# Kernel optimization log

Measured on AMD Instinct MI355X. Metric: run time of the kernel, lower is better.

Reference implementation:

```python
import jax, jax.numpy as jnp
import numpy as np

B, S, E = 4, 1024, 1280
H = 16
D = E // H  # 80


def rotate_half(x):
    x1, x2 = jnp.split(x, 2, axis=-1)
    return jnp.concatenate([-x2, x1], axis=-1)


def setup_inputs() -> dict:
    key = jax.random.key(0)
    ks = jax.random.split(key, 12)
    sc = 0.02
    x = jax.random.normal(ks[0], (B, S, E), dtype=jnp.float32)
    # variable per-item sequence lengths (each <= S), cumulative
    lens = np.array([1024, 896, 768, 640], dtype=np.int32)
    cu_seqlens = jnp.asarray(np.concatenate([[0], np.cumsum(lens)]), dtype=jnp.int32)
    # rotary cos/sin for positions 0..S-1, head_dim D
    inv_freq = 1.0 / (10000.0 ** (np.arange(0, D, 2, dtype=np.float32) / D))
    t = np.arange(S, dtype=np.float32)
    freqs = np.outer(t, inv_freq)               # [S, D/2]
    emb = np.concatenate([freqs, freqs], axis=-1)  # [S, D]
    cos = jnp.asarray(np.cos(emb), dtype=jnp.float32)
    sin = jnp.asarray(np.sin(emb), dtype=jnp.float32)
    wq = jax.random.normal(ks[1], (E, E), dtype=jnp.float32) * sc
    bq = jax.random.normal(ks[2], (E,), dtype=jnp.float32) * sc
    wk = jax.random.normal(ks[3], (E, E), dtype=jnp.float32) * sc
    bk = jax.random.normal(ks[4], (E,), dtype=jnp.float32) * sc
    wv = jax.random.normal(ks[5], (E, E), dtype=jnp.float32) * sc
    bv = jax.random.normal(ks[6], (E,), dtype=jnp.float32) * sc
    wo = jax.random.normal(ks[7], (E, E), dtype=jnp.float32) * sc
    bo = jax.random.normal(ks[8], (E,), dtype=jnp.float32) * sc
    return {"x": x, "cu_seqlens": cu_seqlens, "cos": cos, "sin": sin,
            "wq": wq, "bq": bq, "wk": wk, "bk": bk, "wv": wv, "bv": bv,
            "wo": wo, "bo": bo}


def reference(x, cu_seqlens, cos, sin, wq, bq, wk, bk, wv, bv, wo, bo):
    b, s, e = x.shape
    h, d = H, D
    # QKV projections (nn.Linear: x @ W^T + b)
    q = (x @ wq.T + bq).reshape(b, s, h, d)
    k = (x @ wk.T + bk).reshape(b, s, h, d)
    v = (x @ wv.T + bv).reshape(b, s, h, d)
    # rotary embedding (apply_rotary_pos_emb, 'normal')
    c = cos[None, :, None, :]  # [1, s, 1, d]
    sn = sin[None, :, None, :]
    q = q * c + rotate_half(q) * sn
    k = k * c + rotate_half(k) * sn
    # patch attention mask from cu_seqlens (flatten_batch=False):
    # token i attends to token j iff i < len_b and j < len_b
    seq_lens = cu_seqlens[1:] - cu_seqlens[:-1]          # [b]
    idx = jnp.arange(s)
    valid = idx[None, :] < seq_lens[:, None]             # [b, s]
    mask = valid[:, None, :, None] & valid[:, None, None, :]  # [b, 1, s, s]
    # SDPA, non-causal
    scale = 1.0 / jnp.sqrt(jnp.asarray(d, dtype=q.dtype))
    scores = jnp.einsum("bqhd,bkhd->bhqk", q, k) * scale
    scores = jnp.where(mask, scores, jnp.asarray(-1e9, dtype=scores.dtype))
    attn = jax.nn.softmax(scores, axis=-1)
    out = jnp.einsum("bhqk,bkhd->bqhd", attn, v)         # [b, s, h, d]
    out = out.reshape(b, s, e)
    # output projection
    return out @ wo.T + bo
```

## Files before the change

kernel.cpp:

```cpp
#include <hip/hip_runtime.h>
#include <hip/hip_bf16.h>

#define B_ 4
#define S_ 1024
#define E_ 1280
#define H_ 16
#define D_ 80
#define M_ (B_*S_)
#define QBLK 128

typedef __hip_bfloat16 bf16;
using bf16x8 = __attribute__((ext_vector_type(8))) short;
using f32x4  = __attribute__((ext_vector_type(4))) float;

__device__ __forceinline__ float b2f(bf16 x){ return __bfloat162float(x); }
__device__ __forceinline__ bf16  f2b(float x){ return __float2bfloat16(x); }
__device__ __forceinline__ void  stf(float* p, float v){ *p = v; }
__device__ __forceinline__ void  stf(bf16*  p, float v){ *p = f2b(v); }

__device__ __forceinline__ void gload_lds16(const void* g, void* l) {
    __builtin_amdgcn_global_load_lds(
        (const __attribute__((address_space(1))) unsigned int*)g,
        (__attribute__((address_space(3))) unsigned int*)l, 16, 0, 0);
}

__device__ __forceinline__ void ph_begin() {
    __builtin_amdgcn_s_barrier();
    asm volatile("s_waitcnt lgkmcnt(0)" ::: "memory");
    __builtin_amdgcn_sched_barrier(0);
    __builtin_amdgcn_s_setprio(1);
}
__device__ __forceinline__ void ph_end() {
    __builtin_amdgcn_s_setprio(0);
    __builtin_amdgcn_sched_barrier(0);
    __builtin_amdgcn_s_barrier();
}
__device__ __forceinline__ void ph_end_vm6() {
    __builtin_amdgcn_s_setprio(0);
    __builtin_amdgcn_sched_barrier(0);
    asm volatile("s_waitcnt vmcnt(6)" ::: "memory");
    __builtin_amdgcn_s_barrier();
}
__device__ __forceinline__ void ph_end_vm0() {
    __builtin_amdgcn_s_setprio(0);
    __builtin_amdgcn_sched_barrier(0);
    asm volatile("s_waitcnt vmcnt(0)" ::: "memory");
    __builtin_amdgcn_s_barrier();
}

__global__ __launch_bounds__(256) void cvt_kernel(
    const float* __restrict__ s0, const float* __restrict__ s1,
    const float* __restrict__ s2, const float* __restrict__ s3,
    const float* __restrict__ s4,
    bf16* __restrict__ d0, bf16* __restrict__ d1, bf16* __restrict__ d2,
    bf16* __restrict__ d3, bf16* __restrict__ d4,
    int n0, int n1)
{
    const float* s; bf16* d; int n;
    switch (blockIdx.y) {
        case 0: s = s0; d = d0; n = n0; break;
        case 1: s = s1; d = d1; n = n1; break;
        case 2: s = s2; d = d2; n = n1; break;
        case 3: s = s3; d = d3; n = n1; break;
        default: s = s4; d = d4; n = n1; break;
    }
    int i = (blockIdx.x * 256 + threadIdx.x) * 8;
    if (i >= n) return;
    float4 a = *(const float4*)(s + i);
    float4 b = *(const float4*)(s + i + 4);
    bf16 t[8];
    t[0]=f2b(a.x); t[1]=f2b(a.y); t[2]=f2b(a.z); t[3]=f2b(a.w);
    t[4]=f2b(b.x); t[5]=f2b(b.y); t[6]=f2b(b.z); t[7]=f2b(b.w);
    *(uint4*)(d + i) = *(const uint4*)t;
}

__global__ __launch_bounds__(512, 2) void qkv_gemm_8ph(
    const bf16* __restrict__ A,
    const bf16* __restrict__ W0, const bf16* __restrict__ W1, const bf16* __restrict__ W2,
    const float* __restrict__ b0, const float* __restrict__ b1, const float* __restrict__ b2,
    bf16* __restrict__ Cq, bf16* __restrict__ Ck, bf16* __restrict__ Cv)
{
    constexpr int K = 1280;
    constexpr int NITER = K / 128;

    __shared__ __align__(16) bf16 Asm[2][2][128*64];
    __shared__ __align__(16) bf16 Bsm[2][2][128*64];

    const int bm  = blockIdx.x * 256;
    const int ny  = blockIdx.y;
    const int mat = ny / 5;
    const int bn  = (ny % 5) * 256;
    const bf16*  W    = (mat == 0) ? W0 : (mat == 1) ? W1 : W2;
    const float* bias = (mat == 0) ? b0 : (mat == 1) ? b1 : b2;

    const int tid  = threadIdx.x;
    const int lane = tid & 63, wv = tid >> 6;
    const int wm = wv >> 2, wn = wv & 3;
    const int quad = lane >> 4, l15 = lane & 15;

    auto stageA = [&](int j_, int half) {
        #pragma unroll
        for (int i = 0; i < 2; i++) {
            const int c   = tid + i*512;
            const int row = c >> 3;
            const int g   = (c & 7) ^ (row & 7);
            gload_lds16(A + (size_t)(bm + half*128 + row) * K + j_*64 + g*8,
                        &Asm[j_ & 1][half][(wv*64 + i*512) * 8]);
        }
    };
    auto stageB = [&](int j_, int half) {
        #pragma unroll
        for (int i = 0; i < 2; i++) {
            const int c   = tid + i*512;
            const int row = c >> 3;
            const int g   = (c & 7) ^ (row & 7);
            gload_lds16(W + (size_t)(bn + half*128 + row) * K + j_*64 + g*8,
                        &Bsm[j_ & 1][half][(wv*64 + i*512) * 8]);
        }
    };
    auto lda = [&](int bf, int mt, int ks) -> bf16x8 {
        const int r = mt*16 + l15;
        return *(const bf16x8*)&Asm[bf][wm][r*64 + (((quad + ks*4) ^ (r & 7)) << 3)];
    };
    auto ldb = [&](int bf, int nt, int ks) -> bf16x8 {
        const int r = (wn & 1)*64 + nt*16 + l15;
        return *(const bf16x8*)&Bsm[bf][wn >> 1][r*64 + (((quad + ks*4) ^ (r & 7)) << 3)];
    };

    f32x4 acc[8][4] = {};
    bf16x8 a[4][2], bA[2][2], bB[2][2];

#define MFMA_Q(MT0, NT0, BB_) do { \
    _Pragma("unroll") for (int mt_ = 0; mt_ < 4; mt_++) \
    _Pragma("unroll") for (int nt_ = 0; nt_ < 2; nt_++) \
    _Pragma("unroll") for (int ks_ = 0; ks_ < 2; ks_++) \
        acc[(MT0)+mt_][(NT0)+nt_] = __builtin_amdgcn_mfma_f32_16x16x32_bf16( \
            a[mt_][ks_], BB_[nt_][ks_], acc[(MT0)+mt_][(NT0)+nt_], 0, 0, 0); \
} while (0)

    stageA(0, 0); stageA(0, 1); stageB(0, 0); stageB(0, 1);
    stageA(1, 0); stageA(1, 1); stageB(1, 0); stageB(1, 1);
    __syncthreads();

    for (int t = 0; t < NITER; t++) {
        const int  j  = 2*t;
        const bool pf = (t + 1 < NITER);

        #pragma unroll
        for (int mt = 0; mt < 4; mt++) { a[mt][0] = lda(0, mt, 0); a[mt][1] = lda(0, mt, 1); }
        #pragma unroll
        for (int nt = 0; nt < 2; nt++) { bA[nt][0] = ldb(0, nt, 0); bA[nt][1] = ldb(0, nt, 1); }
        stageA(j+1, 1);
        ph_begin(); MFMA_Q(0, 0, bA); ph_end();

        #pragma unroll
        for (int nt = 0; nt < 2; nt++) { bB[nt][0] = ldb(0, 2+nt, 0); bB[nt][1] = ldb(0, 2+nt, 1); }
        ph_begin(); MFMA_Q(0, 2, bB); ph_end();

        #pragma unroll
        for (int mt = 0; mt < 4; mt++) { a[mt][0] = lda(0, 4+mt, 0); a[mt][1] = lda(0, 4+mt, 1); }
        if (pf) stageB(j+2, 0);
        ph_begin(); MFMA_Q(4, 0, bA); ph_end();

        if (pf) { stageB(j+2, 1); stageA(j+2, 0); }
        ph_begin(); MFMA_Q(4, 2, bB);
        if (pf) ph_end_vm6(); else ph_end_vm0();

        #pragma unroll
        for (int mt = 0; mt < 4; mt++) { a[mt][0] = lda(1, mt, 0); a[mt][1] = lda(1, mt, 1); }
        #pragma unroll
        for (int nt = 0; nt < 2; nt++) { bA[nt][0] = ldb(1, nt, 0); bA[nt][1] = ldb(1, nt, 1); }
        if (pf) stageA(j+2, 1);
        ph_begin(); MFMA_Q(0, 0, bA); ph_end();

        #pragma unroll
        for (int nt = 0; nt < 2; nt++) { bB[nt][0] = ldb(1, 2+nt, 0); bB[nt][1] = ldb(1, 2+nt, 1); }
        ph_begin(); MFMA_Q(0, 2, bB); ph_end();

        #pragma unroll
        for (int mt = 0; mt < 4; mt++) { a[mt][0] = lda(1, 4+mt, 0); a[mt][1] = lda(1, 4+mt, 1); }
        if (pf) stageB(j+3, 0);
        ph_begin(); MFMA_Q(4, 0, bA); ph_end();

        if (pf) { stageB(j+3, 1); stageA(j+3, 0); }
        ph_begin(); MFMA_Q(4, 2, bB); ph_end_vm6();
    }
#undef MFMA_Q

    if (mat < 2) {
        bf16* C = (mat == 0) ? Cq : Ck;
        #pragma unroll
        for (int nt = 0; nt < 4; nt++) {
            const int ncol = bn + wn*64 + nt*16 + l15;
            const float bv = bias[ncol];
            #pragma unroll
            for (int mt = 0; mt < 8; mt++) {
                const int m0 = bm + wm*128 + mt*16 + quad*4;
                #pragma unroll
                for (int r = 0; r < 4; r++)
                    C[(size_t)(m0 + r) * E_ + ncol] = f2b(acc[mt][nt][r] + bv);
            }
        }
    } else {
        #pragma unroll
        for (int nt = 0; nt < 4; nt++) {
            const int ncol = bn + wn*64 + nt*16 + l15;
            const float bv = bias[ncol];
            const int hh = ncol / 80, dd = ncol % 80;
            #pragma unroll
            for (int mt = 0; mt < 8; mt++) {
                const int m0  = bm + wm*128 + mt*16 + quad*4;
                const int btok = m0 >> 10;
                const int key  = m0 & 1023;
                union { bf16 h[4]; uint2 u; } t4;
                #pragma unroll
                for (int r = 0; r < 4; r++) t4.h[r] = f2b(acc[mt][nt][r] + bv);
                *(uint2*)&Cv[((size_t)(btok*H_ + hh)*D_ + dd)*S_ + key] = t4.u;
            }
        }
    }
}

template<typename TC, bool VT_OUT>
__global__ __launch_bounds__(256) void mfma_gemm_bt(
    const bf16* __restrict__ A,
    const bf16* __restrict__ W0, const bf16* __restrict__ W1, const bf16* __restrict__ W2,
    const float* __restrict__ b0, const float* __restrict__ b1, const float* __restrict__ b2,
    TC* __restrict__ C0, TC* __restrict__ C1, TC* __restrict__ C2,
    int K, int N, int ntiles)
{
    const int mat = blockIdx.y / ntiles;
    const int bn  = (blockIdx.y % ntiles) * 128;
    const int bm  = blockIdx.x * 128;
    const bf16* W; const float* bias; TC* C;
    if (mat == 0)      { W = W0; bias = b0; C = C0; }
    else if (mat == 1) { W = W1; bias = b1; C = C1; }
    else               { W = W2; bias = b2; C = C2; }

    __shared__ bf16 As[2][128][32];
    __shared__ bf16 Ws[2][128][32];

    const int tid  = threadIdx.x;
    const int lane = tid & 63;
    const int wv   = tid >> 6;
    const int wm   = (wv & 1) * 64;
    const int wn   = (wv >> 1) * 64;
    const int srow = wv * 16 + (lane >> 2);
    const int scol = (lane & 3) * 8;

    f32x4 acc[4][4] = {};

    for (int k0 = 0; k0 < K; k0 += 64) {
        __syncthreads();
        #pragma unroll
        for (int p = 0; p < 2; p++) {
            const int kc = k0 + p*32 + scol;
            gload_lds16(A + (size_t)(bm + srow)      * K + kc, &As[p][wv*16][0]);
            gload_lds16(A + (size_t)(bm + 64 + srow) * K + kc, &As[p][64 + wv*16][0]);
            gload_lds16(W + (size_t)(bn + srow)      * K + kc, &Ws[p][wv*16][0]);
            gload_lds16(W + (size_t)(bn + 64 + srow) * K + kc, &Ws[p][64 + wv*16][0]);
        }
        __syncthreads();

        const int fr = lane & 15;
        const int kq = (lane >> 4) * 8;
        #pragma unroll
        for (int p = 0; p < 2; p++) {
            bf16x8 af[4], wf[4];
            #pragma unroll
            for (int t = 0; t < 4; t++) {
                af[t] = *(const bf16x8*)&As[p][wm + t*16 + fr][kq];
                wf[t] = *(const bf16x8*)&Ws[p][wn + t*16 + fr][kq];
            }
            #pragma unroll
            for (int mt = 0; mt < 4; mt++)
                #pragma unroll
                for (int nt = 0; nt < 4; nt++)
                    acc[mt][nt] = __builtin_amdgcn_mfma_f32_16x16x32_bf16(
                        af[mt], wf[nt], acc[mt][nt], 0, 0, 0);
        }
    }

    const int col_l = lane & 15;
    const int row_l = (lane >> 4) * 4;

    if (VT_OUT && mat == 2) {
        const int btok = bm >> 10;
        const int keyb = (bm & 1023) + wm + row_l;
        #pragma unroll
        for (int nt = 0; nt < 4; nt++) {
            const int n = bn + wn + nt*16 + col_l;
            const float bv = bias[n];
            const int hh = n / 80, dd = n % 80;
            bf16* vbase = (bf16*)C + ((size_t)(btok*H_ + hh)*D_ + dd)*S_ + keyb;
            #pragma unroll
            for (int mt = 0; mt < 4; mt++) {
                union { bf16 h[4]; uint2 u; } t4;
                #pragma unroll
                for (int r = 0; r < 4; r++) t4.h[r] = f2b(acc[mt][nt][r] + bv);
                *(uint2*)&vbase[mt*16] = t4.u;
            }
        }
    } else {
        #pragma unroll
        for (int nt = 0; nt < 4; nt++) {
            const int n = bn + wn + nt*16 + col_l;
            const float bv = bias[n];
            #pragma unroll
            for (int mt = 0; mt < 4; mt++) {
                #pragma unroll
                for (int r = 0; r < 4; r++) {
                    const int m = bm + wm + mt*16 + row_l + r;
                    stf(&C[(size_t)m * N + n], acc[mt][nt][r] + bv);
                }
            }
        }
    }
}

__device__ __forceinline__ void rope8(const bf16* lo, const bf16* hi,
                                      const float* cp, const float* sp,
                                      float mul, uint4* out_lo, uint4* out_hi)
{
    union { uint4 u; bf16 h[8]; } li, hi_, lo_o, hi_o;
    li.u  = *(const uint4*)lo;
    hi_.u = *(const uint4*)hi;
    #pragma unroll
    for (int u = 0; u < 8; u++) {
        float x1 = b2f(li.h[u]), x2 = b2f(hi_.h[u]);
        float c = cp[u], s = sp[u];
        lo_o.h[u] = f2b((x1*c - x2*s) * mul);
        hi_o.h[u] = f2b((x2*c + x1*s) * mul);
    }
    *out_lo = lo_o.u;
    *out_hi = hi_o.u;
}

__global__ __launch_bounds__(256) void rope_kernel(
    bf16* __restrict__ qp, bf16* __restrict__ kp,
    const float* __restrict__ cosp, const float* __restrict__ sinp)
{
    int idx = blockIdx.x * 256 + threadIdx.x;
    const int NT = M_ * H_ * 5;
    bf16* base; float mul;
    if (idx < NT) { base = qp; mul = 0.11180339887498949f; }
    else         { base = kp; mul = 1.0f; idx -= NT; }
    const int row = idx / 80;
    const int rem = idx - row * 80;
    const int h   = rem / 5;
    const int pc  = rem - h * 5;
    const int s   = row & (S_ - 1);
    bf16* p = base + (size_t)row * E_ + h * D_ + pc * 8;
    const float* cp = cosp + s * D_ + pc * 8;
    const float* sp = sinp + s * D_ + pc * 8;
    uint4 olo, ohi;
    rope8(p, p + 40, cp, sp, mul, &olo, &ohi);
    *(uint4*)p        = olo;
    *(uint4*)(p + 40) = ohi;
}

__global__ __launch_bounds__(512, 4) void attn_mfma(
    const bf16* __restrict__ q, const bf16* __restrict__ k, const bf16* __restrict__ vt,
    const int* __restrict__ cu, bf16* __restrict__ o)
{
    __shared__ __align__(16) bf16 Ks[2][64*80];
    __shared__ __align__(16) bf16 VTs[2][80*64];
    __shared__ __align__(16) bf16 PTs[8][16*76];

    const int n  = blockIdx.x;
    const int g  = ((n >> 6) << 3) | (n & 7);
    const int qs = (n >> 3) & 7;
    const int b  = g >> 4;
    const int h  = g & 15;

    const int tid  = threadIdx.x;
    const int lane = tid & 63, wv = tid >> 6;
    const int quad = lane >> 4, l15 = lane & 15;
    const int q0   = qs * QBLK;
    const int len  = cu[b + 1] - cu[b];

    const bool uniformq = (q0 >= len);
    const bool clean    = ((len & (QBLK - 1)) == 0);
    const int  ktiles   = uniformq ? 16 : (clean ? (len >> 6) : 16);
    const bool domask   = !uniformq && !clean;

    bf16* PT = &PTs[wv][0];

    bf16x8 qf[3] = {};
    if (!uniformq) {
        const bf16* qrow = q + (size_t)(b*S_ + q0 + wv*16 + l15)*E_ + h*D_ + quad*8;
        qf[0] = *(const bf16x8*)(qrow);
        qf[1] = *(const bf16x8*)(qrow + 32);
        if (quad < 2) qf[2] = *(const bf16x8*)(qrow + 64);
    } else {
        const bf16 one = f2b(1.0f);
        #pragma unroll
        for (int nt = 0; nt < 4; nt++)
            #pragma unroll
            for (int r = 0; r < 4; r++)
                PT[(quad*4 + r)*76 + nt*16 + l15] = one;
    }

    float m_r[4], l_r[4];
    #pragma unroll
    for (int r = 0; r < 4; r++) { m_r[r] = -1e30f; l_r[r] = 0.f; }
    f32x4 o_acc[5] = {};

    const int u_  = l15 >> 2;
    const int s0r = quad ^ u_;
    const int sv0 = quad ^ (l15 & 7);

    auto stage = [&](int kt, int bf) {
        #pragma unroll
        for (int i = 0; i < 3; i++) {
            int c = tid + i * 512;
            if (c < 640) {
                if (!uniformq) {
                    int row = c / 10, s5 = c - row * 10;
                    int uu = (row >> 2) & 3;
                    int sg = (s5 < 8) ? (s5 ^ uu) : (8 + ((s5 ^ uu) & 1));
                    gload_lds16(k + (size_t)(b*S_ + kt*64 + row)*E_ + h*D_ + sg*8,
                                &Ks[bf][c*8]);
                }
            } else if (c < 1280) {
                int c2 = c - 640;
                int row = c2 >> 3, s5 = c2 & 7;
                int sg = s5 ^ (row & 7);
                gload_lds16(vt + ((size_t)(b*H_ + h)*D_ + row)*S_ + kt*64 + sg*8,
                            &VTs[bf][c2*8]);
            }
        }
    };

    stage(0, 0);
    __syncthreads();

    const bool q_full = (q0 + 64) <= len;

    for (int kt = 0; kt < ktiles; kt++) {
        const int cur = kt & 1;
        if (kt + 1 < ktiles) stage(kt + 1, cur ^ 1);

        if (!uniformq) {
            f32x4 s4[4];
            #pragma unroll
            for (int nt = 0; nt < 4; nt++) {
                const bf16* kr = &Ks[cur][(nt*16 + l15) * 80];
                bf16x8 kf0 = *(const bf16x8*)(kr + s0r*8);
                bf16x8 kf1 = *(const bf16x8*)(kr + 32 + s0r*8);
                bf16x8 kf2 = {};
                if (quad < 2) kf2 = *(const bf16x8*)(kr + 64 + (s0r & 1)*8);
                f32x4 a0 = {};
                a0 = __builtin_amdgcn_mfma_f32_16x16x32_bf16(qf[0], kf0, a0, 0, 0, 0);
                a0 = __builtin_amdgcn_mfma_f32_16x16x32_bf16(qf[1], kf1, a0, 0, 0, 0);
                a0 = __builtin_amdgcn_mfma_f32_16x16x32_bf16(qf[2], kf2, a0, 0, 0, 0);
                s4[nt] = a0;
            }

            float sv[4][4];
            if (!domask || (q_full && (kt*64 + 64) <= len)) {
                #pragma unroll
                for (int r = 0; r < 4; r++)
                    #pragma unroll
                    for (int nt = 0; nt < 4; nt++)
                        sv[nt][r] = s4[nt][r];
            } else {
                bool vk[4];
                #pragma unroll
                for (int nt = 0; nt < 4; nt++) vk[nt] = (kt*64 + nt*16 + l15) < len;
                #pragma unroll
                for (int r = 0; r < 4; r++) {
                    const bool vq = (q0 + wv*16 + quad*4 + r) < len;
                    #pragma unroll
                    for (int nt = 0; nt < 4; nt++)
                        sv[nt][r] = (vq && vk[nt]) ? s4[nt][r] : -1e9f;
                }
            }
            float rmax[4];
            #pragma unroll
            for (int r = 0; r < 4; r++)
                rmax[r] = fmaxf(fmaxf(sv[0][r], sv[1][r]), fmaxf(sv[2][r], sv[3][r]));
            #pragma unroll
            for (int st = 1; st < 16; st <<= 1)
                #pragma unroll
                for (int r = 0; r < 4; r++)
                    rmax[r] = fmaxf(rmax[r], __shfl_xor(rmax[r], st, 64));
            float mnew[4], alpha[4], rsum[4], p[4][4];
            #pragma unroll
            for (int r = 0; r < 4; r++) {
                mnew[r]  = fmaxf(m_r[r], rmax[r]);
                alpha[r] = __expf(m_r[r] - mnew[r]);
                float a = 0.f;
                #pragma unroll
                for (int nt = 0; nt < 4; nt++) { p[nt][r] = __expf(sv[nt][r] - mnew[r]); a += p[nt][r]; }
                rsum[r] = a;
            }
            #pragma unroll
            for (int st = 1; st < 16; st <<= 1)
                #pragma unroll
                for (int r = 0; r < 4; r++)
                    rsum[r] += __shfl_xor(rsum[r], st, 64);
            #pragma unroll
            for (int r = 0; r < 4; r++) {
                l_r[r] = l_r[r] * alpha[r] + rsum[r];
                m_r[r] = mnew[r];
            }
            #pragma unroll
            for (int dt = 0; dt < 5; dt++)
                #pragma unroll
                for (int r = 0; r < 4; r++)
                    o_acc[dt][r] *= alpha[r];
            #pragma unroll
            for (int nt = 0; nt < 4; nt++)
                #pragma unroll
                for (int r = 0; r < 4; r++)
                    PT[(quad*4 + r)*76 + nt*16 + l15] = f2b(p[nt][r]);
        }

        bf16x8 pa0 = *(const bf16x8*)&PT[l15*76 + quad*8];
        bf16x8 pa1 = *(const bf16x8*)&PT[l15*76 + 32 + quad*8];
        #pragma unroll
        for (int dt = 0; dt < 5; dt++) {
            const bf16* vr = &VTs[cur][(dt*16 + l15) * 64];
            bf16x8 vf0 = *(const bf16x8*)(vr + sv0*8);
            bf16x8 vf1 = *(const bf16x8*)(vr + (sv0 ^ 4)*8);
            o_acc[dt] = __builtin_amdgcn_mfma_f32_16x16x32_bf16(pa0, vf0, o_acc[dt], 0, 0, 0);
            o_acc[dt] = __builtin_amdgcn_mfma_f32_16x16x32_bf16(pa1, vf1, o_acc[dt], 0, 0, 0);
        }
        __syncthreads();
    }

    #pragma unroll
    for (int r = 0; r < 4; r++) {
        const float inv = uniformq ? (1.0f / 1024.0f) : (1.0f / l_r[r]);
        size_t row_g = (size_t)(b*S_ + q0 + wv*16 + quad*4 + r);
        #pragma unroll
        for (int dt = 0; dt < 5; dt++)
            o[row_g*E_ + h*D_ + dt*16 + l15] = f2b(o_acc[dt][r] * inv);
    }
}

extern "C" void kernel_launch(void* const* d_in, const int* in_sizes, int n_in,
                              void* d_out, int out_size, void* d_ws, size_t ws_size,
                              hipStream_t stream)
{
    const float* x    = (const float*)d_in[0];
    const int*   cu   = (const int*)  d_in[1];
    const float* cosp = (const float*)d_in[2];
    const float* sinp = (const float*)d_in[3];
    const float* wq   = (const float*)d_in[4];
    const float* bq   = (const float*)d_in[5];
    const float* wk   = (const float*)d_in[6];
    const float* bk   = (const float*)d_in[7];
    const float* wv   = (const float*)d_in[8];
    const float* bv   = (const float*)d_in[9];
    const float* wo   = (const float*)d_in[10];
    const float* bo   = (const float*)d_in[11];
    float* out = (float*)d_out;

    bf16* q   = (bf16*)d_ws;
    bf16* kk  = q   + (size_t)M_ * E_;
    bf16* vt  = kk  + (size_t)M_ * E_;
    bf16* ao  = vt  + (size_t)M_ * E_;
    bf16* xb  = ao  + (size_t)M_ * E_;
    bf16* wqb = xb  + (size_t)M_ * E_;
    bf16* wkb = wqb + (size_t)E_ * E_;
    bf16* wvb = wkb + (size_t)E_ * E_;
    bf16* wob = wvb + (size_t)E_ * E_;

    cvt_kernel<<<dim3(2560, 5), 256, 0, stream>>>(
        x, wq, wk, wv, wo, xb, wqb, wkb, wvb, wob, M_*E_, E_*E_);

    qkv_gemm_8ph<<<dim3(M_/256, 15), 512, 0, stream>>>(
        xb, wqb, wkb, wvb, bq, bk, bv, q, kk, vt);

    rope_kernel<<<2560, 256, 0, stream>>>(q, kk, cosp, sinp);

    attn_mfma<<<512, 512, 0, stream>>>(q, kk, vt, cu, ao);

    mfma_gemm_bt<float, false><<<dim3(M_/128, 10), 256, 0, stream>>>(
        ao, wob, wob, wob, bo, bo, bo, out, out, out, E_, E_, 10);
}
```

Measured before the change: 254.5 us.

## Transpose attention MFMA operands so each lane owns one query row

Swaps the A/B operands of the QK^T and PV MFMAs so the accumulator holds S^T/O^T. Each lane then owns a single query row, which turns the per-row softmax max/sum reductions from 4 rows times 4 shuffle steps into 2 shuffles on one scalar. P is written to a swizzled 64-wide LDS tile with packed 8-byte stores. Output is stored as packed 4-element vectors, and uniform (fully masked) query blocks use a register constant of ones instead of filling LDS. This reduces the VALU and shuffle work in softmax and the LDS bank conflicts, at the cost of a more intricate swizzle that must stay consistent with the MFMA fragment layout.

```diff
diff --git a/kernel.cpp b/kernel.cpp
--- a/kernel.cpp
+++ b/kernel.cpp
@@ -365,7 +365,7 @@
 {
     __shared__ __align__(16) bf16 Ks[2][64*80];
     __shared__ __align__(16) bf16 VTs[2][80*64];
-    __shared__ __align__(16) bf16 PTs[8][16*76];
+    __shared__ __align__(16) bf16 PTq[8][16*64];
 
     const int n  = blockIdx.x;
     const int g  = ((n >> 6) << 3) | (n & 7);
@@ -384,7 +384,7 @@
     const int  ktiles   = uniformq ? 16 : (clean ? (len >> 6) : 16);
     const bool domask   = !uniformq && !clean;
 
-    bf16* PT = &PTs[wv][0];
+    bf16* PT = &PTq[wv][0];
 
     bf16x8 qf[3] = {};
     if (!uniformq) {
@@ -392,19 +392,17 @@
         qf[0] = *(const bf16x8*)(qrow);
         qf[1] = *(const bf16x8*)(qrow + 32);
         if (quad < 2) qf[2] = *(const bf16x8*)(qrow + 64);
-    } else {
-        const bf16 one = f2b(1.0f);
-        #pragma unroll
-        for (int nt = 0; nt < 4; nt++)
-            #pragma unroll
-            for (int r = 0; r < 4; r++)
-                PT[(quad*4 + r)*76 + nt*16 + l15] = one;
-    }
-
-    float m_r[4], l_r[4];
-    #pragma unroll
-    for (int r = 0; r < 4; r++) { m_r[r] = -1e30f; l_r[r] = 0.f; }
+    }
+
+    float m_s = -1e30f, l_s = 0.f;
     f32x4 o_acc[5] = {};
+
+    bf16x8 pone;
+    {
+        const short one_s = (short)0x3F80;
+        #pragma unroll
+        for (int i = 0; i < 8; i++) pone[i] = one_s;
+    }
 
     const int u_  = l15 >> 2;
     const int s0r = quad ^ u_;
@@ -441,6 +439,7 @@
         const int cur = kt & 1;
         if (kt + 1 < ktiles) stage(kt + 1, cur ^ 1);
 
+        bf16x8 pf0 = pone, pf1 = pone;
         if (!uniformq) {
             f32x4 s4[4];
             #pragma unroll
@@ -451,92 +450,88 @@
                 bf16x8 kf2 = {};
                 if (quad < 2) kf2 = *(const bf16x8*)(kr + 64 + (s0r & 1)*8);
                 f32x4 a0 = {};
-                a0 = __builtin_amdgcn_mfma_f32_16x16x32_bf16(qf[0], kf0, a0, 0, 0, 0);
-                a0 = __builtin_amdgcn_mfma_f32_16x16x32_bf16(qf[1], kf1, a0, 0, 0, 0);
-                a0 = __builtin_amdgcn_mfma_f32_16x16x32_bf16(qf[2], kf2, a0, 0, 0, 0);
+                a0 = __builtin_amdgcn_mfma_f32_16x16x32_bf16(kf0, qf[0], a0, 0, 0, 0);
+                a0 = __builtin_amdgcn_mfma_f32_16x16x32_bf16(kf1, qf[1], a0, 0, 0, 0);
+                a0 = __builtin_amdgcn_mfma_f32_16x16x32_bf16(kf2, qf[2], a0, 0, 0, 0);
                 s4[nt] = a0;
             }
 
             float sv[4][4];
             if (!domask || (q_full && (kt*64 + 64) <= len)) {
                 #pragma unroll
-                for (int r = 0; r < 4; r++)
+                for (int nt = 0; nt < 4; nt++)
                     #pragma unroll
-                    for (int nt = 0; nt < 4; nt++)
+                    for (int r = 0; r < 4; r++)
                         sv[nt][r] = s4[nt][r];
             } else {
-                bool vk[4];
-                #pragma unroll
-                for (int nt = 0; nt < 4; nt++) vk[nt] = (kt*64 + nt*16 + l15) < len;
+                const bool vq = (q0 + wv*16 + l15) < len;
+                #pragma unroll
+                for (int nt = 0; nt < 4; nt++)
+                    #pragma unroll
+                    for (int r = 0; r < 4; r++) {
+                        const bool vk = (kt*64 + nt*16 + quad*4 + r) < len;
+                        sv[nt][r] = (vq && vk) ? s4[nt][r] : -1e9f;
+                    }
+            }
+
+            float rm[4];
+            #pragma unroll
+            for (int nt = 0; nt < 4; nt++)
+                rm[nt] = fmaxf(fmaxf(sv[nt][0], sv[nt][1]), fmaxf(sv[nt][2], sv[nt][3]));
+            float sloc = fmaxf(fmaxf(rm[0], rm[1]), fmaxf(rm[2], rm[3]));
+            sloc = fmaxf(sloc, __shfl_xor(sloc, 16, 64));
+            sloc = fmaxf(sloc, __shfl_xor(sloc, 32, 64));
+            const float mnew  = fmaxf(m_s, sloc);
+            const float alpha = __expf(m_s - mnew);
+            float p[4][4], lsum = 0.f;
+            #pragma unroll
+            for (int nt = 0; nt < 4; nt++)
                 #pragma unroll
                 for (int r = 0; r < 4; r++) {
-                    const bool vq = (q0 + wv*16 + quad*4 + r) < len;
-                    #pragma unroll
-                    for (int nt = 0; nt < 4; nt++)
-                        sv[nt][r] = (vq && vk[nt]) ? s4[nt][r] : -1e9f;
+                    p[nt][r] = __expf(sv[nt][r] - mnew);
+                    lsum += p[nt][r];
                 }
-            }
-            float rmax[4];
-            #pragma unroll
-            for (int r = 0; r < 4; r++)
-                rmax[r] = fmaxf(fmaxf(sv[0][r], sv[1][r]), fmaxf(sv[2][r], sv[3][r]));
-            #pragma unroll
-            for (int st = 1; st < 16; st <<= 1)
+            lsum += __shfl_xor(lsum, 16, 64);
+            lsum += __shfl_xor(lsum, 32, 64);
+            l_s = l_s * alpha + lsum;
+            m_s = mnew;
+            #pragma unroll
+            for (int dt = 0; dt < 5; dt++)
                 #pragma unroll
                 for (int r = 0; r < 4; r++)
-                    rmax[r] = fmaxf(rmax[r], __shfl_xor(rmax[r], st, 64));
-            float mnew[4], alpha[4], rsum[4], p[4][4];
-            #pragma unroll
-            for (int r = 0; r < 4; r++) {
-                mnew[r]  = fmaxf(m_r[r], rmax[r]);
-                alpha[r] = __expf(m_r[r] - mnew[r]);
-                float a = 0.f;
-                #pragma unroll
-                for (int nt = 0; nt < 4; nt++) { p[nt][r] = __expf(sv[nt][r] - mnew[r]); a += p[nt][r]; }
-                rsum[r] = a;
-            }
-            #pragma unroll
-            for (int st = 1; st < 16; st <<= 1)
-                #pragma unroll
-                for (int r = 0; r < 4; r++)
-                    rsum[r] += __shfl_xor(rsum[r], st, 64);
-            #pragma unroll
-            for (int r = 0; r < 4; r++) {
-                l_r[r] = l_r[r] * alpha[r] + rsum[r];
-                m_r[r] = mnew[r];
-            }
-            #pragma unroll
-            for (int dt = 0; dt < 5; dt++)
-                #pragma unroll
-                for (int r = 0; r < 4; r++)
-                    o_acc[dt][r] *= alpha[r];
-            #pragma unroll
-            for (int nt = 0; nt < 4; nt++)
-                #pragma unroll
-                for (int r = 0; r < 4; r++)
-                    PT[(quad*4 + r)*76 + nt*16 + l15] = f2b(p[nt][r]);
-        }
-
-        bf16x8 pa0 = *(const bf16x8*)&PT[l15*76 + quad*8];
-        bf16x8 pa1 = *(const bf16x8*)&PT[l15*76 + 32 + quad*8];
+                    o_acc[dt][r] *= alpha;
+
+            #pragma unroll
+            for (int nt = 0; nt < 4; nt++) {
+                union { bf16 hh[4]; uint2 u; } w;
+                #pragma unroll
+                for (int r = 0; r < 4; r++) w.hh[r] = f2b(p[nt][r]);
+                const int gw = (2*nt + (quad >> 1)) ^ (l15 & 7);
+                *(uint2*)&PT[l15*64 + gw*8 + (quad & 1)*4] = w.u;
+            }
+            pf0 = *(const bf16x8*)&PT[l15*64 + ((quad    ) ^ (l15 & 7))*8];
+            pf1 = *(const bf16x8*)&PT[l15*64 + ((quad + 4) ^ (l15 & 7))*8];
+        }
+
         #pragma unroll
         for (int dt = 0; dt < 5; dt++) {
             const bf16* vr = &VTs[cur][(dt*16 + l15) * 64];
             bf16x8 vf0 = *(const bf16x8*)(vr + sv0*8);
             bf16x8 vf1 = *(const bf16x8*)(vr + (sv0 ^ 4)*8);
-            o_acc[dt] = __builtin_amdgcn_mfma_f32_16x16x32_bf16(pa0, vf0, o_acc[dt], 0, 0, 0);
-            o_acc[dt] = __builtin_amdgcn_mfma_f32_16x16x32_bf16(pa1, vf1, o_acc[dt], 0, 0, 0);
+            o_acc[dt] = __builtin_amdgcn_mfma_f32_16x16x32_bf16(vf0, pf0, o_acc[dt], 0, 0, 0);
+            o_acc[dt] = __builtin_amdgcn_mfma_f32_16x16x32_bf16(vf1, pf1, o_acc[dt], 0, 0, 0);
         }
         __syncthreads();
     }
 
+    const float inv = uniformq ? (1.0f / 1024.0f) : (1.0f / l_s);
+    const size_t row_g = (size_t)(b*S_ + q0 + wv*16 + l15);
     #pragma unroll
-    for (int r = 0; r < 4; r++) {
-        const float inv = uniformq ? (1.0f / 1024.0f) : (1.0f / l_r[r]);
-        size_t row_g = (size_t)(b*S_ + q0 + wv*16 + quad*4 + r);
-        #pragma unroll
-        for (int dt = 0; dt < 5; dt++)
-            o[row_g*E_ + h*D_ + dt*16 + l15] = f2b(o_acc[dt][r] * inv);
+    for (int dt = 0; dt < 5; dt++) {
+        union { bf16 hh[4]; uint2 u; } t4;
+        #pragma unroll
+        for (int r = 0; r < 4; r++) t4.hh[r] = f2b(o_acc[dt][r] * inv);
+        *(uint2*)&o[row_g*E_ + h*D_ + dt*16 + quad*4] = t4.u;
     }
 }
 
```

Result: faster. 230.8 us (-9.3%).
